# Kernel optimization log

Hardware: AMD Instinct MI355X
Metric: run time of the kernel (lower is better)

The kernel has to match this reference:

```python
import jax, jax.numpy as jnp
import numpy as np

B, S, D, H, FF = 2, 2048, 1024, 16, 4096
DH = D // H  # 64
EPS = 1e-5


def setup_inputs() -> dict:
    key = jax.random.key(0)
    ks = jax.random.split(key, 16)
    s = 0.02
    x = jax.random.normal(ks[0], (B, S, D), dtype=jnp.float32)
    p = jnp.arange(B * S, dtype=jnp.int32).reshape(B, S)
    # RoPE freqs: 32 base freqs padded already to dim_head//2, then cat([f, -f])
    base = 10000.0 ** (-jnp.arange(DH // 2, dtype=jnp.float32) / (DH // 2))
    freqs = jnp.concatenate([base, -base], axis=0)  # [DH]
    return {
        "x": x,
        "p": p,
        "Wqkv": jax.random.normal(ks[1], (3 * D, D), dtype=jnp.float32) * s,
        "bqkv": jnp.zeros((3 * D,), jnp.float32),
        "Wo": jax.random.normal(ks[2], (D, D), dtype=jnp.float32) * s,
        "bo": jnp.zeros((D,), jnp.float32),
        "g_attn": jnp.ones((D,), jnp.float32),
        "b_attn": jnp.zeros((D,), jnp.float32),
        "W1": jax.random.normal(ks[3], (2 * FF, D), dtype=jnp.float32) * s,
        "b1": jnp.zeros((2 * FF,), jnp.float32),
        "W2": jax.random.normal(ks[4], (D, FF), dtype=jnp.float32) * s,
        "b2": jnp.zeros((D,), jnp.float32),
        "g_mlp": jnp.ones((D,), jnp.float32),
        "b_mlp": jnp.zeros((D,), jnp.float32),
        "freqs": freqs,
    }


def _layernorm(x, g, b):
    mu = jnp.mean(x, axis=-1, keepdims=True)
    var = jnp.mean(jnp.square(x - mu), axis=-1, keepdims=True)
    return (x - mu) * jax.lax.rsqrt(var + EPS) * g + b


def _rotate_half(x):
    x1, x2 = jnp.split(x, 2, axis=-1)
    return jnp.concatenate([x2, x1], axis=-1)


def reference(x, p, Wqkv, bqkv, Wo, bo, g_attn, b_attn, W1, b1, W2, b2, g_mlp, b_mlp, freqs):
    # --- self attention ---
    qkv = x @ Wqkv.T + bqkv                      # [B,S,3D]
    qkv = qkv.reshape(B, S, 3, H, DH).transpose(0, 3, 2, 1, 4)  # [B,H,3,S,DH]
    q, k, v = qkv[:, :, 0], qkv[:, :, 1], qkv[:, :, 2]          # [B,H,S,DH]
    # rotary positional encoding (cos/sin are constants w.r.t. grads)
    ang = p.astype(jnp.float32)[:, None, :, None] * freqs       # [B,1,S,DH]
    cos, sin = jnp.cos(ang), jnp.sin(ang)
    q = q * cos + _rotate_half(q) * sin
    k = k * cos + _rotate_half(k) * sin
    scale = DH ** -0.5
    scores = jnp.einsum("bhqd,bhkd->bhqk", q, k) * scale
    attn = jax.nn.softmax(scores, axis=-1)
    o = jnp.einsum("bhqk,bhkd->bhqd", attn, v)                  # [B,H,S,DH]
    o = o.transpose(0, 2, 1, 3).reshape(B, S, D)
    attn_out = o @ Wo.T + bo
    h = _layernorm(attn_out + x, g_attn, b_attn)
    # --- gated MLP (dropout = identity in eval) ---
    u = h @ W1.T + b1                                            # [B,S,2FF]
    a, gate = jnp.split(u, 2, axis=-1)
    m = jax.nn.gelu(a, approximate=False) * gate
    m = m @ W2.T + b2
    return _layernorm(m + h, g_mlp, b_mlp)
```

## Files before the change

kernel.cpp:

```cpp
#include <hip/hip_runtime.h>
#include <stdint.h>


typedef unsigned short u16;
typedef unsigned int u32;
typedef __attribute__((ext_vector_type(8))) __bf16 bf16x8;
typedef __attribute__((ext_vector_type(4))) float f32x4;
typedef __attribute__((ext_vector_type(8))) unsigned short u16x8;

#define MFMA16(a, b, c) __builtin_amdgcn_mfma_f32_16x16x32_bf16(a, b, c, 0, 0, 0)

__device__ __forceinline__ float b2f(u16 u) {
  union { u32 i; float f; } x; x.i = ((u32)u) << 16; return x.f;
}
__device__ __forceinline__ u16 f2b(float f) {
  u32 x = __float_as_uint(f);
  x += 0x7fffu + ((x >> 16) & 1u);
  return (u16)(x >> 16);
}
__device__ __forceinline__ u16 f2b_trunc(float f) {
  return (u16)(__float_as_uint(f) >> 16);
}
__device__ __forceinline__ void stage8(int f32, const void* base, size_t eo, u16* lds) {
  if (f32) {
    const float* s = (const float*)base + eo;
    const float4 a = *(const float4*)s;
    const float4 b = *(const float4*)(s + 4);
    u16x8 o;
    o[0] = f2b(a.x); o[1] = f2b(a.y); o[2] = f2b(a.z); o[3] = f2b(a.w);
    o[4] = f2b(b.x); o[5] = f2b(b.y); o[6] = f2b(b.z); o[7] = f2b(b.w);
    *(u16x8*)lds = o;
  } else {
    *(u16x8*)lds = *(const u16x8*)((const u16*)base + eo);
  }
}
__device__ __forceinline__ float ldsc(int f32, const void* p, size_t i) {
  return f32 ? ((const float*)p)[i] : b2f(((const u16*)p)[i]);
}
__device__ __forceinline__ void gload_lds16(const u16* g, u16* l) {
  __builtin_amdgcn_global_load_lds(
      (__attribute__((address_space(1))) unsigned int*)(unsigned long long)(uintptr_t)g,
      (__attribute__((address_space(3))) unsigned int*)(unsigned int)(uintptr_t)l,
      16, 0, 0);
}
__device__ __forceinline__ float gelu_exact(float a) {
  return 0.5f * a * (1.0f + erff(a * 0.70710678118654752f));
}

__global__ void flag_kernel(const void* g_attn, u32* flag) {
  if (threadIdx.x == 0 && blockIdx.x == 0) {
    flag[0] = (((const u32*)g_attn)[0] == 0x3F800000u) ? 1u : 0u;
    flag[1] = 0u;
  }
}

__global__ __launch_bounds__(256) void conv5_kernel(
    const u32* __restrict__ flagp, const void* __restrict__ s0,
    const void* __restrict__ s1, const void* __restrict__ s2,
    const void* __restrict__ s3, const void* __restrict__ s4,
    u16* __restrict__ out) {
  const int i = (blockIdx.x * 256 + threadIdx.x) * 8;
  const void* src; int off;
  if (i < 7340032) {
    if (i < 4194304) { src = s0; off = i; }
    else             { src = s1; off = i - 4194304; }
  } else if (i < 8388608)  { src = s2; off = i - 7340032; }
  else if (i < 16777216)   { src = s3; off = i - 8388608; }
  else                     { src = s4; off = i - 16777216; }
  if (*flagp) {
    const float* s = (const float*)src + off;
    const float4 a = *(const float4*)s;
    const float4 b = *(const float4*)(s + 4);
    u16x8 o;
    o[0] = f2b(a.x); o[1] = f2b(a.y); o[2] = f2b(a.z); o[3] = f2b(a.w);
    o[4] = f2b(b.x); o[5] = f2b(b.y); o[6] = f2b(b.z); o[7] = f2b(b.w);
    *(u16x8*)(out + i) = o;
  } else {
    *(u16x8*)(out + i) = *(const u16x8*)((const u16*)src + off);
  }
}

__global__ __launch_bounds__(256) void gemm_f(
    const u32* __restrict__ flagp, const u16* __restrict__ A,
    const u16* __restrict__ W, const void* __restrict__ bias,
    u16* __restrict__ out, int M, int N, int K) {
  const int f = (int)*flagp;
  __shared__ __align__(16) u16 a_sm[2][128 * 32];
  __shared__ __align__(16) u16 w_sm[2][128 * 32];
  const int t = threadIdx.x;
  const int lane = t & 63;
  const int quad = lane >> 4, l16 = lane & 15;
  const int wv = t >> 6;
  const int m0 = blockIdx.y * 128, n0 = blockIdx.x * 128;
  const int wm = (wv >> 1) * 64, wn = (wv & 1) * 64;
  f32x4 acc[4][4] = {};

  const int co = (((t & 3) ^ ((t >> 3) & 3)) * 8);
  const int qs = ((quad ^ ((l16 >> 1) & 3)) * 8);
  const u16* aA = A + (size_t)(m0 + (t >> 2)) * K + co;
  const u16* aW = W + (size_t)(n0 + (t >> 2)) * K + co;
  const size_t skip = (size_t)64 * K;

  for (int k0 = 0; k0 < K; k0 += 64) {
    gload_lds16(aA + k0,             &a_sm[0][t * 8]);
    gload_lds16(aA + skip + k0,      &a_sm[0][t * 8 + 2048]);
    gload_lds16(aA + k0 + 32,        &a_sm[1][t * 8]);
    gload_lds16(aA + skip + k0 + 32, &a_sm[1][t * 8 + 2048]);
    gload_lds16(aW + k0,             &w_sm[0][t * 8]);
    gload_lds16(aW + skip + k0,      &w_sm[0][t * 8 + 2048]);
    gload_lds16(aW + k0 + 32,        &w_sm[1][t * 8]);
    gload_lds16(aW + skip + k0 + 32, &w_sm[1][t * 8 + 2048]);
    __syncthreads();
#pragma unroll
    for (int hh = 0; hh < 2; hh++) {
      bf16x8 af[4], wf[4];
#pragma unroll
      for (int i = 0; i < 4; i++)
        af[i] = *(const bf16x8*)&a_sm[hh][(wm + i * 16 + l16) * 32 + qs];
#pragma unroll
      for (int i = 0; i < 4; i++)
        wf[i] = *(const bf16x8*)&w_sm[hh][(wn + i * 16 + l16) * 32 + qs];
#pragma unroll
      for (int mi = 0; mi < 4; mi++)
#pragma unroll
        for (int ni = 0; ni < 4; ni++)
          acc[mi][ni] = MFMA16(af[mi], wf[ni], acc[mi][ni]);
    }
    __syncthreads();
  }

#pragma unroll
  for (int ni = 0; ni < 4; ni++) {
    const int col = n0 + wn + ni * 16 + l16;
    const float bv = ldsc(f, bias, col);
#pragma unroll
    for (int mi = 0; mi < 4; mi++) {
#pragma unroll
      for (int r = 0; r < 4; r++) {
        const int row = m0 + wm + mi * 16 + quad * 4 + r;
        out[(size_t)row * N + col] = f2b(acc[mi][ni][r] + bv);
      }
    }
  }
}

__global__ __launch_bounds__(512, 4) void w1_geglu_f(
    const u32* __restrict__ flagp, const u16* __restrict__ h,
    const u16* __restrict__ W1, const void* __restrict__ b1,
    u16* __restrict__ m) {
  const int f = (int)*flagp;
  const int K = 1024;
  __shared__ __align__(16) u16 a_sm[2][128 * 32];
  __shared__ __align__(16) u16 wa_sm[2][128 * 32];
  __shared__ __align__(16) u16 wg_sm[2][128 * 32];
  const int t = threadIdx.x;
  const int lane = t & 63;
  const int quad = lane >> 4, l16 = lane & 15;
  const int wv = t >> 6;
  const int m0 = blockIdx.y * 128, n0 = blockIdx.x * 128;
  const int wm = (wv >> 2) * 64, wn = (wv & 3) * 32;
  f32x4 acca[4][2] = {}, accg[4][2] = {};

  const int co = (((t & 3) ^ ((t >> 3) & 3)) * 8);
  const int qs = ((quad ^ ((l16 >> 1) & 3)) * 8);
  const u16* aA = h + (size_t)(m0 + (t >> 2)) * K + co;
  const u16* aWa = W1 + (size_t)(n0 + (t >> 2)) * K + co;
  const u16* aWg = W1 + (size_t)(4096 + n0 + (t >> 2)) * K + co;

  for (int k0 = 0; k0 < K; k0 += 64) {
    gload_lds16(aA + k0,       &a_sm[0][t * 8]);
    gload_lds16(aA + k0 + 32,  &a_sm[1][t * 8]);
    gload_lds16(aWa + k0,      &wa_sm[0][t * 8]);
    gload_lds16(aWa + k0 + 32, &wa_sm[1][t * 8]);
    gload_lds16(aWg + k0,      &wg_sm[0][t * 8]);
    gload_lds16(aWg + k0 + 32, &wg_sm[1][t * 8]);
    __syncthreads();
#pragma unroll
    for (int hh = 0; hh < 2; hh++) {
      bf16x8 af[4], waf[2], wgf[2];
#pragma unroll
      for (int i = 0; i < 4; i++)
        af[i] = *(const bf16x8*)&a_sm[hh][(wm + i * 16 + l16) * 32 + qs];
#pragma unroll
      for (int i = 0; i < 2; i++) {
        waf[i] = *(const bf16x8*)&wa_sm[hh][(wn + i * 16 + l16) * 32 + qs];
        wgf[i] = *(const bf16x8*)&wg_sm[hh][(wn + i * 16 + l16) * 32 + qs];
      }
#pragma unroll
      for (int mi = 0; mi < 4; mi++)
#pragma unroll
        for (int ni = 0; ni < 2; ni++) {
          acca[mi][ni] = MFMA16(af[mi], waf[ni], acca[mi][ni]);
          accg[mi][ni] = MFMA16(af[mi], wgf[ni], accg[mi][ni]);
        }
    }
    __syncthreads();
  }

#pragma unroll
  for (int ni = 0; ni < 2; ni++) {
    const int col = n0 + wn + ni * 16 + l16;
    const float ba = ldsc(f, b1, col);
    const float bg = ldsc(f, b1, col + 4096);
#pragma unroll
    for (int mi = 0; mi < 4; mi++) {
#pragma unroll
      for (int r = 0; r < 4; r++) {
        const int row = m0 + wm + mi * 16 + quad * 4 + r;
        const float a = acca[mi][ni][r] + ba;
        const float g = accg[mi][ni][r] + bg;
        m[(size_t)row * 4096 + col] = f2b(gelu_exact(a) * g);
      }
    }
  }
}

__global__ __launch_bounds__(256) void gemm_splitk_f(
    const u16* __restrict__ A, const u16* __restrict__ W,
    float* __restrict__ pk, int M, int N, int Ktot) {
  const int Kh = Ktot >> 1;
  const int z = blockIdx.z;
  __shared__ __align__(16) u16 a_sm[2][128 * 32];
  __shared__ __align__(16) u16 w_sm[2][128 * 32];
  const int t = threadIdx.x;
  const int lane = t & 63;
  const int quad = lane >> 4, l16 = lane & 15;
  const int wv = t >> 6;
  const int m0 = blockIdx.y * 128, n0 = blockIdx.x * 128;
  const int wm = (wv >> 1) * 64, wn = (wv & 1) * 64;
  f32x4 acc[4][4] = {};

  const int co = (((t & 3) ^ ((t >> 3) & 3)) * 8);
  const int qs = ((quad ^ ((l16 >> 1) & 3)) * 8);
  const u16* aA = A + (size_t)(m0 + (t >> 2)) * Ktot + z * Kh + co;
  const u16* aW = W + (size_t)(n0 + (t >> 2)) * Ktot + z * Kh + co;
  const size_t skip = (size_t)64 * Ktot;

  for (int k0 = 0; k0 < Kh; k0 += 64) {
    gload_lds16(aA + k0,             &a_sm[0][t * 8]);
    gload_lds16(aA + skip + k0,      &a_sm[0][t * 8 + 2048]);
    gload_lds16(aA + k0 + 32,        &a_sm[1][t * 8]);
    gload_lds16(aA + skip + k0 + 32, &a_sm[1][t * 8 + 2048]);
    gload_lds16(aW + k0,             &w_sm[0][t * 8]);
    gload_lds16(aW + skip + k0,      &w_sm[0][t * 8 + 2048]);
    gload_lds16(aW + k0 + 32,        &w_sm[1][t * 8]);
    gload_lds16(aW + skip + k0 + 32, &w_sm[1][t * 8 + 2048]);
    __syncthreads();
#pragma unroll
    for (int hh = 0; hh < 2; hh++) {
      bf16x8 af[4], wf[4];
#pragma unroll
      for (int i = 0; i < 4; i++)
        af[i] = *(const bf16x8*)&a_sm[hh][(wm + i * 16 + l16) * 32 + qs];
#pragma unroll
      for (int i = 0; i < 4; i++)
        wf[i] = *(const bf16x8*)&w_sm[hh][(wn + i * 16 + l16) * 32 + qs];
#pragma unroll
      for (int mi = 0; mi < 4; mi++)
#pragma unroll
        for (int ni = 0; ni < 4; ni++)
          acc[mi][ni] = MFMA16(af[mi], wf[ni], acc[mi][ni]);
    }
    __syncthreads();
  }

  float* po = pk + (size_t)z * M * N;
#pragma unroll
  for (int ni = 0; ni < 4; ni++) {
    const int col = n0 + wn + ni * 16 + l16;
#pragma unroll
    for (int mi = 0; mi < 4; mi++) {
#pragma unroll
      for (int r = 0; r < 4; r++) {
        const int row = m0 + wm + mi * 16 + quad * 4 + r;
        po[(size_t)row * N + col] = acc[mi][ni][r];
      }
    }
  }
}

__global__ __launch_bounds__(256) void reduce2_kernel(
    const u32* __restrict__ flagp, const float* __restrict__ pk,
    const void* __restrict__ bias, u16* __restrict__ out, int MN, int N) {
  const int f = (int)*flagp;
  const int i = (blockIdx.x * 256 + threadIdx.x) * 8;
  if (i >= MN) return;
  const float4 a0 = *(const float4*)(pk + i);
  const float4 a1 = *(const float4*)(pk + i + 4);
  const float4 b0 = *(const float4*)(pk + MN + i);
  const float4 b1 = *(const float4*)(pk + MN + i + 4);
  float v[8] = {a0.x + b0.x, a0.y + b0.y, a0.z + b0.z, a0.w + b0.w,
                a1.x + b1.x, a1.y + b1.y, a1.z + b1.z, a1.w + b1.w};
  u16x8 o;
#pragma unroll
  for (int j = 0; j < 8; j++)
    o[j] = f2b(v[j] + ldsc(f, bias, (i + j) & (N - 1)));
  *(u16x8*)(out + i) = o;
}

__global__ __launch_bounds__(256) void qkv_f(
    const u32* __restrict__ flagp, const u16* __restrict__ x,
    const u16* __restrict__ Wq, const void* __restrict__ bq,
    const int* __restrict__ p, const void* __restrict__ freqs,
    u16* __restrict__ qb, u16* __restrict__ kb, u16* __restrict__ vtb) {
  const int f = (int)*flagp;
  const int K = 1024;
  __shared__ __align__(16) u16 a_sm[2][128 * 32];
  __shared__ __align__(16) u16 w_sm[2][128 * 32];
  const int t = threadIdx.x;
  const int lane = t & 63;
  const int quad = lane >> 4, l16 = lane & 15;
  const int wv = t >> 6;
  const int m0 = blockIdx.y * 128, n0 = blockIdx.x * 128;
  const int wm = (wv >> 1) * 64, wn = (wv & 1) * 64;
  f32x4 acc[4][4] = {};

  const int co = (((t & 3) ^ ((t >> 3) & 3)) * 8);
  const int qs = ((quad ^ ((l16 >> 1) & 3)) * 8);
  const u16* aA = x + (size_t)(m0 + (t >> 2)) * K + co;
  const u16* aW = Wq + (size_t)(n0 + (t >> 2)) * K + co;
  const size_t skip = (size_t)64 * K;

  for (int k0 = 0; k0 < K; k0 += 64) {
    gload_lds16(aA + k0,             &a_sm[0][t * 8]);
    gload_lds16(aA + skip + k0,      &a_sm[0][t * 8 + 2048]);
    gload_lds16(aA + k0 + 32,        &a_sm[1][t * 8]);
    gload_lds16(aA + skip + k0 + 32, &a_sm[1][t * 8 + 2048]);
    gload_lds16(aW + k0,             &w_sm[0][t * 8]);
    gload_lds16(aW + skip + k0,      &w_sm[0][t * 8 + 2048]);
    gload_lds16(aW + k0 + 32,        &w_sm[1][t * 8]);
    gload_lds16(aW + skip + k0 + 32, &w_sm[1][t * 8 + 2048]);
    __syncthreads();
#pragma unroll
    for (int hh = 0; hh < 2; hh++) {
      bf16x8 af[4], wf[4];
#pragma unroll
      for (int i = 0; i < 4; i++)
        af[i] = *(const bf16x8*)&a_sm[hh][(wm + i * 16 + l16) * 32 + qs];
#pragma unroll
      for (int i = 0; i < 4; i++)
        wf[i] = *(const bf16x8*)&w_sm[hh][(wn + i * 16 + l16) * 32 + qs];
#pragma unroll
      for (int mi = 0; mi < 4; mi++)
#pragma unroll
        for (int ni = 0; ni < 4; ni++)
          acc[mi][ni] = MFMA16(af[mi], wf[ni], acc[mi][ni]);
    }
    __syncthreads();
  }

  const int nbase = n0 + wn;
  const int type = nbase >> 10;
  const int head = (nbase & 1023) >> 6;
  float bb[4];
#pragma unroll
  for (int ni = 0; ni < 4; ni++) bb[ni] = ldsc(f, bq, nbase + ni * 16 + l16);
  float fr0 = 0.f, fr1 = 0.f;
  if (type < 2) { fr0 = ldsc(f, freqs, l16); fr1 = ldsc(f, freqs, 16 + l16); }

#pragma unroll
  for (int mi = 0; mi < 4; mi++) {
#pragma unroll
    for (int r = 0; r < 4; r++) {
      const int mrow = m0 + wm + mi * 16 + quad * 4 + r;
      const int b = mrow >> 11, s = mrow & 2047;
      if (type < 2) {
        u16* dst = (type == 0 ? qb : kb) + ((size_t)(b * 16 + head) * 2048 + s) * 64;
        const float pm = (float)p[mrow];
#pragma unroll
        for (int ni = 0; ni < 2; ni++) {
          const int d = ni * 16 + l16;
          const float v1 = acc[mi][ni][r] + bb[ni];
          const float v2 = acc[mi][ni + 2][r] + bb[ni + 2];
          const float ang = pm * (ni == 0 ? fr0 : fr1);
          float sn, cs;
          __sincosf(ang, &sn, &cs);
          dst[d]      = f2b(v1 * cs + v2 * sn);
          dst[d + 32] = f2b(v2 * cs - v1 * sn);
        }
      } else {
#pragma unroll
        for (int ni = 0; ni < 4; ni++) {
          const int d = ni * 16 + l16;
          vtb[((size_t)(b * 16 + head) * 64 + d) * 2048 + s] = f2b(acc[mi][ni][r] + bb[ni]);
        }
      }
    }
  }
}

__global__ __launch_bounds__(256) void attn_kernel(
    const u16* __restrict__ q, const u16* __restrict__ k,
    const u16* __restrict__ vt, u16* __restrict__ o) {
  __shared__ __align__(16) u16 k_sm[2][64 * 64];
  __shared__ __align__(16) u16 v_sm[2][64 * 64];
  __shared__ __align__(16) u16 p_sm[4 * 32 * 72];
  const int t = threadIdx.x;
  const int lane = t & 63, w = t >> 6;
  const int quad = lane >> 4, l16 = lane & 15;
  const int fid = blockIdx.x;
  const int bh = (fid & 7) + ((fid >> 7) << 3);
  const int qt = (fid >> 3) & 15;
  const size_t base = (size_t)bh * 2048 * 64;

  const int cs[2] = {((quad ^ (l16 & 7)) * 8), (((4 + quad) ^ (l16 & 7)) * 8)};
  u16* pw = &p_sm[w * 32 * 72];

  bf16x8 qf[2][2];
#pragma unroll
  for (int mi = 0; mi < 2; mi++) {
    const u16* qp = q + base + (size_t)(qt * 128 + w * 32 + mi * 16 + l16) * 64 + quad * 8;
    qf[mi][0] = *(const bf16x8*)qp;
    qf[mi][1] = *(const bf16x8*)(qp + 32);
  }
  f32x4 o_acc[2][4] = {};
  float l_i[8];
#pragma unroll
  for (int i = 0; i < 8; i++) l_i[i] = 0.f;

  const int r0 = t >> 3, sc0 = ((t & 7) ^ ((t >> 3) & 7)) * 8;
  const int c1 = t + 256;
  const int r1 = c1 >> 3, sc1 = ((c1 & 7) ^ ((c1 >> 3) & 7)) * 8;

  for (int kt = 0; kt < 16; ++kt) {
    const u16* kg = k + base + (size_t)kt * 128 * 64;
    const u16* vg = vt + base + (size_t)kt * 128;
    gload_lds16(kg + (size_t)r0 * 64 + sc0,        &k_sm[0][t * 8]);
    gload_lds16(kg + (size_t)r1 * 64 + sc1,        &k_sm[0][c1 * 8]);
    gload_lds16(kg + (size_t)(64 + r0) * 64 + sc0, &k_sm[1][t * 8]);
    gload_lds16(kg + (size_t)(64 + r1) * 64 + sc1, &k_sm[1][c1 * 8]);
    gload_lds16(vg + (size_t)r0 * 2048 + sc0,      &v_sm[0][t * 8]);
    gload_lds16(vg + (size_t)r1 * 2048 + sc1,      &v_sm[0][c1 * 8]);
    gload_lds16(vg + (size_t)r0 * 2048 + 64 + sc0, &v_sm[1][t * 8]);
    gload_lds16(vg + (size_t)r1 * 2048 + 64 + sc1, &v_sm[1][c1 * 8]);
    __syncthreads();

#pragma unroll
    for (int hh = 0; hh < 2; hh++) {
      f32x4 s_acc[2][4] = {};
#pragma unroll
      for (int kk = 0; kk < 2; kk++) {
#pragma unroll
        for (int ni = 0; ni < 4; ni++) {
          bf16x8 kf = *(const bf16x8*)&k_sm[hh][(ni * 16 + l16) * 64 + cs[kk]];
#pragma unroll
          for (int mi = 0; mi < 2; mi++)
            s_acc[mi][ni] = MFMA16(qf[mi][kk], kf, s_acc[mi][ni]);
        }
      }

#pragma unroll
      for (int mi = 0; mi < 2; mi++) {
#pragma unroll
        for (int r = 0; r < 4; r++) {
          const int ri = mi * 4 + r;
          float sv[4];
#pragma unroll
          for (int ni = 0; ni < 4; ni++)
            sv[ni] = __expf(fmaf(s_acc[mi][ni][r], 0.125f, -8.0f));
          float rs = (sv[0] + sv[1]) + (sv[2] + sv[3]);
#pragma unroll
          for (int msk = 1; msk < 16; msk <<= 1) rs += __shfl_xor(rs, msk);
          l_i[ri] += rs;
#pragma unroll
          for (int ni = 0; ni < 4; ni++)
            pw[(mi * 16 + quad * 4 + r) * 72 + ni * 16 + l16] = f2b_trunc(sv[ni]);
        }
      }

#pragma unroll
      for (int kk = 0; kk < 2; kk++) {
        bf16x8 pf[2];
#pragma unroll
        for (int mi = 0; mi < 2; mi++)
          pf[mi] = *(const bf16x8*)&pw[(mi * 16 + l16) * 72 + kk * 32 + quad * 8];
#pragma unroll
        for (int ni = 0; ni < 4; ni++) {
          bf16x8 vf = *(const bf16x8*)&v_sm[hh][(ni * 16 + l16) * 64 + cs[kk]];
#pragma unroll
          for (int mi = 0; mi < 2; mi++)
            o_acc[mi][ni] = MFMA16(pf[mi], vf, o_acc[mi][ni]);
        }
      }
    }
    __syncthreads();
  }

  const int b = bh >> 4, h = bh & 15;
#pragma unroll
  for (int mi = 0; mi < 2; mi++) {
#pragma unroll
    for (int r = 0; r < 4; r++) {
      const float inv = 1.0f / l_i[mi * 4 + r];
      const int srow = qt * 128 + w * 32 + mi * 16 + quad * 4 + r;
      u16* op = o + ((size_t)(b * 2048 + srow)) * 1024 + h * 64;
#pragma unroll
      for (int ni = 0; ni < 4; ni++) op[ni * 16 + l16] = f2b(o_acc[mi][ni][r] * inv);
    }
  }
}

__global__ __launch_bounds__(256) void gemm_kernel(
    const u32* __restrict__ flagp, const u16* __restrict__ A,
    const void* __restrict__ W, const void* __restrict__ bias,
    u16* __restrict__ out, int M, int N, int K) {
  const int f = (int)*flagp;
  __shared__ __align__(16) u16 a_sm[128 * 32];
  __shared__ __align__(16) u16 w_sm[128 * 32];
  const int t = threadIdx.x;
  const int lane = t & 63;
  const int quad = lane >> 4, l16 = lane & 15;
  const int wv = t >> 6;
  const int m0 = blockIdx.y * 128, n0 = blockIdx.x * 128;
  const int wm = (wv >> 1) * 64, wn = (wv & 1) * 64;
  f32x4 acc[4][4] = {};

  const size_t arow = (size_t)(m0 + (t >> 2)) * K + (t & 3) * 8;
  const size_t wrow = (size_t)(n0 + (t >> 2)) * K + (t & 3) * 8;
  const size_t skip = (size_t)64 * K;

  for (int k0 = 0; k0 < K; k0 += 32) {
    *(u16x8*)&a_sm[t * 8] = *(const u16x8*)(A + arow + k0);
    *(u16x8*)&a_sm[t * 8 + 2048] = *(const u16x8*)(A + arow + skip + k0);
    stage8(f, W, wrow + k0, &w_sm[t * 8]);
    stage8(f, W, wrow + skip + k0, &w_sm[t * 8 + 2048]);
    __syncthreads();
    bf16x8 af[4], wf[4];
#pragma unroll
    for (int i = 0; i < 4; i++)
      af[i] = *(const bf16x8*)&a_sm[(wm + i * 16 + l16) * 32 + quad * 8];
#pragma unroll
    for (int i = 0; i < 4; i++)
      wf[i] = *(const bf16x8*)&w_sm[(wn + i * 16 + l16) * 32 + quad * 8];
#pragma unroll
    for (int mi = 0; mi < 4; mi++)
#pragma unroll
      for (int ni = 0; ni < 4; ni++)
        acc[mi][ni] = MFMA16(af[mi], wf[ni], acc[mi][ni]);
    __syncthreads();
  }

#pragma unroll
  for (int ni = 0; ni < 4; ni++) {
    const int col = n0 + wn + ni * 16 + l16;
    const float bv = ldsc(f, bias, col);
#pragma unroll
    for (int mi = 0; mi < 4; mi++) {
#pragma unroll
      for (int r = 0; r < 4; r++) {
        const int row = m0 + wm + mi * 16 + quad * 4 + r;
        out[(size_t)row * N + col] = f2b(acc[mi][ni][r] + bv);
      }
    }
  }
}

__global__ __launch_bounds__(256) void qkv_kernel(
    const u32* __restrict__ flagp, const void* __restrict__ x,
    const void* __restrict__ Wq, const void* __restrict__ bq,
    const int* __restrict__ p, const void* __restrict__ freqs,
    u16* __restrict__ qb, u16* __restrict__ kb, u16* __restrict__ vtb) {
  const int f = (int)*flagp;
  const int K = 1024;
  __shared__ __align__(16) u16 a_sm[128 * 32];
  __shared__ __align__(16) u16 w_sm[128 * 32];
  const int t = threadIdx.x;
  const int lane = t & 63;
  const int quad = lane >> 4, l16 = lane & 15;
  const int wv = t >> 6;
  const int m0 = blockIdx.y * 128, n0 = blockIdx.x * 128;
  const int wm = (wv >> 1) * 64, wn = (wv & 1) * 64;
  f32x4 acc[4][4] = {};

  const size_t arow = (size_t)(m0 + (t >> 2)) * K + (t & 3) * 8;
  const size_t wrow = (size_t)(n0 + (t >> 2)) * K + (t & 3) * 8;
  const size_t skip = (size_t)64 * K;

  for (int k0 = 0; k0 < K; k0 += 32) {
    stage8(f, x, arow + k0, &a_sm[t * 8]);
    stage8(f, x, arow + skip + k0, &a_sm[t * 8 + 2048]);
    stage8(f, Wq, wrow + k0, &w_sm[t * 8]);
    stage8(f, Wq, wrow + skip + k0, &w_sm[t * 8 + 2048]);
    __syncthreads();
    bf16x8 af[4], wf[4];
#pragma unroll
    for (int i = 0; i < 4; i++)
      af[i] = *(const bf16x8*)&a_sm[(wm + i * 16 + l16) * 32 + quad * 8];
#pragma unroll
    for (int i = 0; i < 4; i++)
      wf[i] = *(const bf16x8*)&w_sm[(wn + i * 16 + l16) * 32 + quad * 8];
#pragma unroll
    for (int mi = 0; mi < 4; mi++)
#pragma unroll
      for (int ni = 0; ni < 4; ni++)
        acc[mi][ni] = MFMA16(af[mi], wf[ni], acc[mi][ni]);
    __syncthreads();
  }

  const int nbase = n0 + wn;
  const int type = nbase >> 10;
  const int head = (nbase & 1023) >> 6;
  float bb[4];
#pragma unroll
  for (int ni = 0; ni < 4; ni++) bb[ni] = ldsc(f, bq, nbase + ni * 16 + l16);
  float fr0 = 0.f, fr1 = 0.f;
  if (type < 2) { fr0 = ldsc(f, freqs, l16); fr1 = ldsc(f, freqs, 16 + l16); }

#pragma unroll
  for (int mi = 0; mi < 4; mi++) {
#pragma unroll
    for (int r = 0; r < 4; r++) {
      const int mrow = m0 + wm + mi * 16 + quad * 4 + r;
      const int b = mrow >> 11, s = mrow & 2047;
      if (type < 2) {
        u16* dst = (type == 0 ? qb : kb) + ((size_t)(b * 16 + head) * 2048 + s) * 64;
        const float pm = (float)p[mrow];
#pragma unroll
        for (int ni = 0; ni < 2; ni++) {
          const int d = ni * 16 + l16;
          const float v1 = acc[mi][ni][r] + bb[ni];
          const float v2 = acc[mi][ni + 2][r] + bb[ni + 2];
          const float ang = pm * (ni == 0 ? fr0 : fr1);
          float sn, cs;
          __sincosf(ang, &sn, &cs);
          dst[d]      = f2b(v1 * cs + v2 * sn);
          dst[d + 32] = f2b(v2 * cs - v1 * sn);
        }
      } else {
#pragma unroll
        for (int ni = 0; ni < 4; ni++) {
          const int d = ni * 16 + l16;
          vtb[((size_t)(b * 16 + head) * 64 + d) * 2048 + s] = f2b(acc[mi][ni][r] + bb[ni]);
        }
      }
    }
  }
}

__global__ __launch_bounds__(256) void w1_geglu_kernel(
    const u32* __restrict__ flagp, const u16* __restrict__ h,
    const void* __restrict__ W1, const void* __restrict__ b1,
    u16* __restrict__ m) {
  const int f = (int)*flagp;
  const int K = 1024;
  __shared__ __align__(16) u16 a_sm[128 * 32];
  __shared__ __align__(16) u16 wa_sm[128 * 32];
  __shared__ __align__(16) u16 wg_sm[128 * 32];
  const int t = threadIdx.x;
  const int lane = t & 63;
  const int quad = lane >> 4, l16 = lane & 15;
  const int wv = t >> 6;
  const int m0 = blockIdx.y * 128, n0 = blockIdx.x * 128;
  const int wm = (wv >> 1) * 64, wn = (wv & 1) * 64;
  f32x4 acca[4][4] = {}, accg[4][4] = {};

  const size_t arow = (size_t)(m0 + (t >> 2)) * K + (t & 3) * 8;
  const size_t warow = (size_t)(n0 + (t >> 2)) * K + (t & 3) * 8;
  const size_t wgrow = (size_t)(4096 + n0 + (t >> 2)) * K + (t & 3) * 8;
  const size_t skip = (size_t)64 * K;

  for (int k0 = 0; k0 < K; k0 += 32) {
    *(u16x8*)&a_sm[t * 8] = *(const u16x8*)(h + arow + k0);
    *(u16x8*)&a_sm[t * 8 + 2048] = *(const u16x8*)(h + arow + skip + k0);
    stage8(f, W1, warow + k0, &wa_sm[t * 8]);
    stage8(f, W1, warow + skip + k0, &wa_sm[t * 8 + 2048]);
    stage8(f, W1, wgrow + k0, &wg_sm[t * 8]);
    stage8(f, W1, wgrow + skip + k0, &wg_sm[t * 8 + 2048]);
    __syncthreads();
    bf16x8 af[4], waf[4], wgf[4];
#pragma unroll
    for (int i = 0; i < 4; i++) {
      af[i]  = *(const bf16x8*)&a_sm[(wm + i * 16 + l16) * 32 + quad * 8];
      waf[i] = *(const bf16x8*)&wa_sm[(wn + i * 16 + l16) * 32 + quad * 8];
      wgf[i] = *(const bf16x8*)&wg_sm[(wn + i * 16 + l16) * 32 + quad * 8];
    }
#pragma unroll
    for (int mi = 0; mi < 4; mi++)
#pragma unroll
      for (int ni = 0; ni < 4; ni++) {
        acca[mi][ni] = MFMA16(af[mi], waf[ni], acca[mi][ni]);
        accg[mi][ni] = MFMA16(af[mi], wgf[ni], accg[mi][ni]);
      }
    __syncthreads();
  }

#pragma unroll
  for (int ni = 0; ni < 4; ni++) {
    const int col = n0 + wn + ni * 16 + l16;
    const float ba = ldsc(f, b1, col);
    const float bg = ldsc(f, b1, col + 4096);
#pragma unroll
    for (int mi = 0; mi < 4; mi++) {
#pragma unroll
      for (int r = 0; r < 4; r++) {
        const int row = m0 + wm + mi * 16 + quad * 4 + r;
        const float a = acca[mi][ni][r] + ba;
        const float g = accg[mi][ni][r] + bg;
        m[(size_t)row * 4096 + col] = f2b(gelu_exact(a) * g);
      }
    }
  }
}

__global__ __launch_bounds__(256) void lnfuse_kernel(
    const u32* __restrict__ flagp, const u16* __restrict__ a,
    const void* __restrict__ b, int b_ext, const void* __restrict__ g,
    const void* __restrict__ bb, void* __restrict__ out, int out_ext) {
  const int f = (int)*flagp;
  const int fb = f & b_ext, fo = f & out_ext;
  const int row = blockIdx.x, t = threadIdx.x;
  float v[4];
#pragma unroll
  for (int i = 0; i < 4; i++) {
    const size_t idx = (size_t)row * 1024 + t * 4 + i;
    v[i] = b2f(a[idx]) + ldsc(fb, b, idx);
  }
  float s = v[0] + v[1] + v[2] + v[3];
  float ss = v[0] * v[0] + v[1] * v[1] + v[2] * v[2] + v[3] * v[3];
#pragma unroll
  for (int msk = 1; msk < 64; msk <<= 1) {
    s += __shfl_xor(s, msk);
    ss += __shfl_xor(ss, msk);
  }
  __shared__ float red[8];
  const int lane = t & 63, wv = t >> 6;
  if (lane == 0) { red[wv] = s; red[wv + 4] = ss; }
  __syncthreads();
  const float S = red[0] + red[1] + red[2] + red[3];
  const float SS = red[4] + red[5] + red[6] + red[7];
  const float mean = S * (1.f / 1024.f);
  const float var = SS * (1.f / 1024.f) - mean * mean;
  const float rstd = rsqrtf(fmaxf(var, 0.f) + 1e-5f);
#pragma unroll
  for (int i = 0; i < 4; i++) {
    const size_t idx = (size_t)row * 1024 + t * 4 + i;
    const float o = (v[i] - mean) * rstd * ldsc(f, g, t * 4 + i) + ldsc(f, bb, t * 4 + i);
    if (fo) ((float*)out)[idx] = o;
    else    ((u16*)out)[idx] = f2b(o);
  }
}

extern "C" void kernel_launch(void* const* d_in, const int* in_sizes, int n_in,
                              void* d_out, int out_size, void* d_ws, size_t ws_size,
                              hipStream_t stream) {
  const void* x      = d_in[0];
  const int*  p      = (const int*)d_in[1];
  const void* Wqkv   = d_in[2];
  const void* bqkv   = d_in[3];
  const void* Wo     = d_in[4];
  const void* bo     = d_in[5];
  const void* g_attn = d_in[6];
  const void* b_attn = d_in[7];
  const void* W1     = d_in[8];
  const void* b1     = d_in[9];
  const void* W2     = d_in[10];
  const void* b2     = d_in[11];
  const void* g_mlp  = d_in[12];
  const void* b_mlp  = d_in[13];
  const void* freqs  = d_in[14];

  char* ws = (char*)d_ws;
  const size_t MB = 1ull << 20;
  const bool fast = ws_size >= 88 * MB + 4096;

  if (fast) {
    u16* xb   = (u16*)(ws + 0 * MB);
    u16* Wqb  = (u16*)(ws + 8 * MB);
    u16* Wob  = (u16*)(ws + 14 * MB);
    u16* W1b  = (u16*)(ws + 16 * MB);
    u16* W2b  = (u16*)(ws + 32 * MB);
    u16* qb   = (u16*)(ws + 40 * MB);
    u16* kb   = (u16*)(ws + 48 * MB);
    u16* vtb  = (u16*)(ws + 56 * MB);
    u16* ob   = (u16*)(ws + 64 * MB);
    u16* ua   = (u16*)(ws + 56 * MB);
    float* pk = (float*)(ws + 0 * MB);
    u16* ao   = qb;
    u16* hb   = kb;
    u16* m2   = qb;
    u32* flg  = (u32*)(ws + 88 * MB);

    flag_kernel<<<1, 64, 0, stream>>>(g_attn, flg);
    conv5_kernel<<<10240, 256, 0, stream>>>(flg, x, Wqkv, Wo, W1, W2, (u16*)ws);

    qkv_f<<<dim3(24, 32), 256, 0, stream>>>(flg, xb, Wqb, bqkv, p, freqs, qb, kb, vtb);
    attn_kernel<<<512, 256, 0, stream>>>(qb, kb, vtb, ob);
    gemm_f<<<dim3(8, 32), 256, 0, stream>>>(flg, ob, Wob, bo, ao, 4096, 1024, 1024);
    lnfuse_kernel<<<4096, 256, 0, stream>>>(flg, ao, x, 1, g_attn, b_attn, hb, 0);
    w1_geglu_f<<<dim3(32, 32), 512, 0, stream>>>(flg, hb, W1b, b1, ua);
    gemm_splitk_f<<<dim3(8, 32, 2), 256, 0, stream>>>(ua, W2b, pk, 4096, 1024, 4096);
    reduce2_kernel<<<2048, 256, 0, stream>>>(flg, pk, b2, m2, 4194304, 1024);
    lnfuse_kernel<<<4096, 256, 0, stream>>>(flg, m2, hb, 0, g_mlp, b_mlp, d_out, 1);
  } else {
    u16* qb  = (u16*)(ws + 0 * MB);
    u16* kb  = (u16*)(ws + 8 * MB);
    u16* vtb = (u16*)(ws + 16 * MB);
    u16* ob  = (u16*)(ws + 24 * MB);
    u16* ao  = (u16*)(ws + 0 * MB);
    u16* hb  = (u16*)(ws + 8 * MB);
    u16* mq  = (u16*)(ws + 16 * MB);
    u16* m2  = (u16*)(ws + 24 * MB);
    u32* flg = (u32*)(ws + 32 * MB);

    flag_kernel<<<1, 64, 0, stream>>>(g_attn, flg);
    qkv_kernel<<<dim3(24, 32), 256, 0, stream>>>(flg, x, Wqkv, bqkv, p, freqs,
                                                 qb, kb, vtb);
    attn_kernel<<<512, 256, 0, stream>>>(qb, kb, vtb, ob);
    gemm_kernel<<<dim3(8, 32), 256, 0, stream>>>(flg, ob, Wo, bo, ao, 4096, 1024, 1024);
    lnfuse_kernel<<<4096, 256, 0, stream>>>(flg, ao, x, 1, g_attn, b_attn, hb, 0);
    for (int quar = 0; quar < 4; quar++) {
      const size_t ro = (size_t)quar * 1024;
      w1_geglu_kernel<<<dim3(32, 8), 256, 0, stream>>>(flg, hb + ro * 1024, W1, b1, mq);
      gemm_kernel<<<dim3(8, 8), 256, 0, stream>>>(flg, mq, W2, b2, m2 + ro * 1024,
                                                  1024, 1024, 4096);
    }
    lnfuse_kernel<<<4096, 256, 0, stream>>>(flg, m2, hb, 0, g_mlp, b_mlp, d_out, 1);
  }
}
```

Before: 455.9 us.

## Use 128x64 GEMM tiles for Wo and W2, drop split-K, defer softmax row-sum shuffles

Replaces the 128x128 Wo GEMM and the split-K W2 GEMM plus its reduce kernel with a single 128x64-tile GEMM that launches twice as many blocks. This removes the fp32 partial write/read and one kernel launch, and gives better CU occupancy on the N=1024 outputs. In attention, the per-tile cross-lane row-sum shuffles are moved to a single reduction after the loop, and s_setprio is placed around the MFMA sections. The smaller tiles lower reuse per block, and the W2 GEMM now runs its full K=4096 in one block, which lengthens that kernel's tail.

```diff
diff --git a/kernel.cpp b/kernel.cpp
--- a/kernel.cpp
+++ b/kernel.cpp
@@ -80,20 +80,21 @@
   }
 }
 
-__global__ __launch_bounds__(256) void gemm_f(
+
+__global__ __launch_bounds__(256) void gemm_n64_f(
     const u32* __restrict__ flagp, const u16* __restrict__ A,
     const u16* __restrict__ W, const void* __restrict__ bias,
     u16* __restrict__ out, int M, int N, int K) {
   const int f = (int)*flagp;
   __shared__ __align__(16) u16 a_sm[2][128 * 32];
-  __shared__ __align__(16) u16 w_sm[2][128 * 32];
+  __shared__ __align__(16) u16 w_sm[2][64 * 32];
   const int t = threadIdx.x;
   const int lane = t & 63;
   const int quad = lane >> 4, l16 = lane & 15;
   const int wv = t >> 6;
-  const int m0 = blockIdx.y * 128, n0 = blockIdx.x * 128;
-  const int wm = (wv >> 1) * 64, wn = (wv & 1) * 64;
-  f32x4 acc[4][4] = {};
+  const int m0 = blockIdx.y * 128, n0 = blockIdx.x * 64;
+  const int wm = (wv >> 1) * 64, wn = (wv & 1) * 32;
+  f32x4 acc[4][2] = {};
 
   const int co = (((t & 3) ^ ((t >> 3) & 3)) * 8);
   const int qs = ((quad ^ ((l16 >> 1) & 3)) * 8);
@@ -107,30 +108,28 @@
     gload_lds16(aA + k0 + 32,        &a_sm[1][t * 8]);
     gload_lds16(aA + skip + k0 + 32, &a_sm[1][t * 8 + 2048]);
     gload_lds16(aW + k0,             &w_sm[0][t * 8]);
-    gload_lds16(aW + skip + k0,      &w_sm[0][t * 8 + 2048]);
     gload_lds16(aW + k0 + 32,        &w_sm[1][t * 8]);
-    gload_lds16(aW + skip + k0 + 32, &w_sm[1][t * 8 + 2048]);
     __syncthreads();
 #pragma unroll
     for (int hh = 0; hh < 2; hh++) {
-      bf16x8 af[4], wf[4];
+      bf16x8 af[4], wf[2];
 #pragma unroll
       for (int i = 0; i < 4; i++)
         af[i] = *(const bf16x8*)&a_sm[hh][(wm + i * 16 + l16) * 32 + qs];
 #pragma unroll
-      for (int i = 0; i < 4; i++)
+      for (int i = 0; i < 2; i++)
         wf[i] = *(const bf16x8*)&w_sm[hh][(wn + i * 16 + l16) * 32 + qs];
 #pragma unroll
       for (int mi = 0; mi < 4; mi++)
 #pragma unroll
-        for (int ni = 0; ni < 4; ni++)
+        for (int ni = 0; ni < 2; ni++)
           acc[mi][ni] = MFMA16(af[mi], wf[ni], acc[mi][ni]);
     }
     __syncthreads();
   }
 
 #pragma unroll
-  for (int ni = 0; ni < 4; ni++) {
+  for (int ni = 0; ni < 2; ni++) {
     const int col = n0 + wn + ni * 16 + l16;
     const float bv = ldsc(f, bias, col);
 #pragma unroll
@@ -215,89 +214,6 @@
   }
 }
 
-__global__ __launch_bounds__(256) void gemm_splitk_f(
-    const u16* __restrict__ A, const u16* __restrict__ W,
-    float* __restrict__ pk, int M, int N, int Ktot) {
-  const int Kh = Ktot >> 1;
-  const int z = blockIdx.z;
-  __shared__ __align__(16) u16 a_sm[2][128 * 32];
-  __shared__ __align__(16) u16 w_sm[2][128 * 32];
-  const int t = threadIdx.x;
-  const int lane = t & 63;
-  const int quad = lane >> 4, l16 = lane & 15;
-  const int wv = t >> 6;
-  const int m0 = blockIdx.y * 128, n0 = blockIdx.x * 128;
-  const int wm = (wv >> 1) * 64, wn = (wv & 1) * 64;
-  f32x4 acc[4][4] = {};
-
-  const int co = (((t & 3) ^ ((t >> 3) & 3)) * 8);
-  const int qs = ((quad ^ ((l16 >> 1) & 3)) * 8);
-  const u16* aA = A + (size_t)(m0 + (t >> 2)) * Ktot + z * Kh + co;
-  const u16* aW = W + (size_t)(n0 + (t >> 2)) * Ktot + z * Kh + co;
-  const size_t skip = (size_t)64 * Ktot;
-
-  for (int k0 = 0; k0 < Kh; k0 += 64) {
-    gload_lds16(aA + k0,             &a_sm[0][t * 8]);
-    gload_lds16(aA + skip + k0,      &a_sm[0][t * 8 + 2048]);
-    gload_lds16(aA + k0 + 32,        &a_sm[1][t * 8]);
-    gload_lds16(aA + skip + k0 + 32, &a_sm[1][t * 8 + 2048]);
-    gload_lds16(aW + k0,             &w_sm[0][t * 8]);
-    gload_lds16(aW + skip + k0,      &w_sm[0][t * 8 + 2048]);
-    gload_lds16(aW + k0 + 32,        &w_sm[1][t * 8]);
-    gload_lds16(aW + skip + k0 + 32, &w_sm[1][t * 8 + 2048]);
-    __syncthreads();
-#pragma unroll
-    for (int hh = 0; hh < 2; hh++) {
-      bf16x8 af[4], wf[4];
-#pragma unroll
-      for (int i = 0; i < 4; i++)
-        af[i] = *(const bf16x8*)&a_sm[hh][(wm + i * 16 + l16) * 32 + qs];
-#pragma unroll
-      for (int i = 0; i < 4; i++)
-        wf[i] = *(const bf16x8*)&w_sm[hh][(wn + i * 16 + l16) * 32 + qs];
-#pragma unroll
-      for (int mi = 0; mi < 4; mi++)
-#pragma unroll
-        for (int ni = 0; ni < 4; ni++)
-          acc[mi][ni] = MFMA16(af[mi], wf[ni], acc[mi][ni]);
-    }
-    __syncthreads();
-  }
-
-  float* po = pk + (size_t)z * M * N;
-#pragma unroll
-  for (int ni = 0; ni < 4; ni++) {
-    const int col = n0 + wn + ni * 16 + l16;
-#pragma unroll
-    for (int mi = 0; mi < 4; mi++) {
-#pragma unroll
-      for (int r = 0; r < 4; r++) {
-        const int row = m0 + wm + mi * 16 + quad * 4 + r;
-        po[(size_t)row * N + col] = acc[mi][ni][r];
-      }
-    }
-  }
-}
-
-__global__ __launch_bounds__(256) void reduce2_kernel(
-    const u32* __restrict__ flagp, const float* __restrict__ pk,
-    const void* __restrict__ bias, u16* __restrict__ out, int MN, int N) {
-  const int f = (int)*flagp;
-  const int i = (blockIdx.x * 256 + threadIdx.x) * 8;
-  if (i >= MN) return;
-  const float4 a0 = *(const float4*)(pk + i);
-  const float4 a1 = *(const float4*)(pk + i + 4);
-  const float4 b0 = *(const float4*)(pk + MN + i);
-  const float4 b1 = *(const float4*)(pk + MN + i + 4);
-  float v[8] = {a0.x + b0.x, a0.y + b0.y, a0.z + b0.z, a0.w + b0.w,
-                a1.x + b1.x, a1.y + b1.y, a1.z + b1.z, a1.w + b1.w};
-  u16x8 o;
-#pragma unroll
-  for (int j = 0; j < 8; j++)
-    o[j] = f2b(v[j] + ldsc(f, bias, (i + j) & (N - 1)));
-  *(u16x8*)(out + i) = o;
-}
-
 __global__ __launch_bounds__(256) void qkv_f(
     const u32* __restrict__ flagp, const u16* __restrict__ x,
     const u16* __restrict__ Wq, const void* __restrict__ bq,
@@ -438,6 +354,7 @@
 #pragma unroll
     for (int hh = 0; hh < 2; hh++) {
       f32x4 s_acc[2][4] = {};
+      __builtin_amdgcn_s_setprio(1);
 #pragma unroll
       for (int kk = 0; kk < 2; kk++) {
 #pragma unroll
@@ -448,6 +365,7 @@
             s_acc[mi][ni] = MFMA16(qf[mi][kk], kf, s_acc[mi][ni]);
         }
       }
+      __builtin_amdgcn_s_setprio(0);
 
 #pragma unroll
       for (int mi = 0; mi < 2; mi++) {
@@ -458,16 +376,14 @@
 #pragma unroll
           for (int ni = 0; ni < 4; ni++)
             sv[ni] = __expf(fmaf(s_acc[mi][ni][r], 0.125f, -8.0f));
-          float rs = (sv[0] + sv[1]) + (sv[2] + sv[3]);
-#pragma unroll
-          for (int msk = 1; msk < 16; msk <<= 1) rs += __shfl_xor(rs, msk);
-          l_i[ri] += rs;
+          l_i[ri] += (sv[0] + sv[1]) + (sv[2] + sv[3]);
 #pragma unroll
           for (int ni = 0; ni < 4; ni++)
             pw[(mi * 16 + quad * 4 + r) * 72 + ni * 16 + l16] = f2b_trunc(sv[ni]);
         }
       }
 
+      __builtin_amdgcn_s_setprio(1);
 #pragma unroll
       for (int kk = 0; kk < 2; kk++) {
         bf16x8 pf[2];
@@ -482,8 +398,15 @@
             o_acc[mi][ni] = MFMA16(pf[mi], vf, o_acc[mi][ni]);
         }
       }
-    }
-    __syncthreads();
+      __builtin_amdgcn_s_setprio(0);
+    }
+    __syncthreads();
+  }
+
+#pragma unroll
+  for (int ri = 0; ri < 8; ri++) {
+#pragma unroll
+    for (int msk = 1; msk < 16; msk <<= 1) l_i[ri] += __shfl_xor(l_i[ri], msk);
   }
 
   const int b = bh >> 4, h = bh & 15;
@@ -774,7 +697,6 @@
     u16* vtb  = (u16*)(ws + 56 * MB);
     u16* ob   = (u16*)(ws + 64 * MB);
     u16* ua   = (u16*)(ws + 56 * MB);
-    float* pk = (float*)(ws + 0 * MB);
     u16* ao   = qb;
     u16* hb   = kb;
     u16* m2   = qb;
@@ -785,11 +707,10 @@
 
     qkv_f<<<dim3(24, 32), 256, 0, stream>>>(flg, xb, Wqb, bqkv, p, freqs, qb, kb, vtb);
     attn_kernel<<<512, 256, 0, stream>>>(qb, kb, vtb, ob);
-    gemm_f<<<dim3(8, 32), 256, 0, stream>>>(flg, ob, Wob, bo, ao, 4096, 1024, 1024);
+    gemm_n64_f<<<dim3(16, 32), 256, 0, stream>>>(flg, ob, Wob, bo, ao, 4096, 1024, 1024);
     lnfuse_kernel<<<4096, 256, 0, stream>>>(flg, ao, x, 1, g_attn, b_attn, hb, 0);
     w1_geglu_f<<<dim3(32, 32), 512, 0, stream>>>(flg, hb, W1b, b1, ua);
-    gemm_splitk_f<<<dim3(8, 32, 2), 256, 0, stream>>>(ua, W2b, pk, 4096, 1024, 4096);
-    reduce2_kernel<<<2048, 256, 0, stream>>>(flg, pk, b2, m2, 4194304, 1024);
+    gemm_n64_f<<<dim3(16, 32), 256, 0, stream>>>(flg, ua, W2b, b2, m2, 4096, 1024, 4096);
     lnfuse_kernel<<<4096, 256, 0, stream>>>(flg, m2, hb, 0, g_mlp, b_mlp, d_out, 1);
   } else {
     u16* qb  = (u16*)(ws + 0 * MB);
```

Result: faster. 437.8 us (-4.0%).
